# Optimization experiments

Hardware: AMD Instinct MI355X
Metric: run time of the kernel (lower is better)

Reference implementation:

```python
import jax, jax.numpy as jnp
import numpy as np

H = 16  # hidden_dim
EPS = 1e-5


def _lstm_layer(x, W_ih, W_hh, b_ih, b_hh):
    # x: [B,T,D_in] -> [B,T,H]; PyTorch gate order i,f,g,o
    B = x.shape[0]
    xg = jnp.einsum('btd,gd->btg', x, W_ih) + (b_ih + b_hh)  # [B,T,4H]

    def step(carry, xt):
        h, c = carry
        gates = xt + h @ W_hh.T
        i, f, g, o = jnp.split(gates, 4, axis=-1)
        c = jax.nn.sigmoid(f) * c + jax.nn.sigmoid(i) * jnp.tanh(g)
        h = jax.nn.sigmoid(o) * jnp.tanh(c)
        return (h, c), h

    h0 = jnp.zeros((B, H), x.dtype)
    _, hs = jax.lax.scan(step, (h0, h0), jnp.swapaxes(xg, 0, 1))  # [T,B,H]
    return jnp.swapaxes(hs, 0, 1)


def setup_inputs() -> dict:
    key = jax.random.key(0)
    ks = jax.random.split(key, 20)
    B, T, D, O = 256, 2048, 57, 4
    x = jax.random.normal(ks[0], (B, T, D), dtype=jnp.float32)
    lengths = jnp.maximum(jnp.sort(jax.random.randint(ks[1], (B,), 1, T + 1))[::-1], 1)
    s = 1.0 / np.sqrt(H)
    u = lambda k, shp: jax.random.uniform(k, shp, jnp.float32, -s, s)
    inp = {'x': x, 'lengths': lengths}
    dims_in = [D, H, H]
    for l in range(3):
        inp[f'W_ih{l}'] = u(ks[2 + 4 * l], (4 * H, dims_in[l]))
        inp[f'W_hh{l}'] = u(ks[3 + 4 * l], (4 * H, H))
        inp[f'b_ih{l}'] = u(ks[4 + 4 * l], (4 * H,))
        inp[f'b_hh{l}'] = u(ks[5 + 4 * l], (4 * H,))
    inp['bn_gamma'] = jnp.ones((H,), jnp.float32)
    inp['bn_beta'] = jnp.zeros((H,), jnp.float32)
    inp['fc_w'] = u(ks[14], (O, H))
    inp['fc_b'] = u(ks[15], (O,))
    return inp


def reference(x, lengths, W_ih0, W_hh0, b_ih0, b_hh0, W_ih1, W_hh1, b_ih1, b_hh1,
              W_ih2, W_hh2, b_ih2, b_hh2, bn_gamma, bn_beta, fc_w, fc_b):
    B, T, _ = x.shape
    h = x
    for W_ih, W_hh, b_ih, b_hh in ((W_ih0, W_hh0, b_ih0, b_hh0),
                                    (W_ih1, W_hh1, b_ih1, b_hh1),
                                    (W_ih2, W_hh2, b_ih2, b_hh2)):
        h = _lstm_layer(h, W_ih, W_hh, b_ih, b_hh)
    # pad_packed_sequence: zero out positions past each sequence length
    mask = (jnp.arange(T)[None, :] < lengths[:, None])[:, :, None].astype(h.dtype)
    h = h * mask  # [B,T,H]
    # BatchNorm1d (training mode) over (batch,time) per channel, incl. padding zeros
    mean = jnp.mean(h, axis=(0, 1))
    var = jnp.mean((h - mean) ** 2, axis=(0, 1))
    norm = (h - mean) * jax.lax.rsqrt(var + EPS) * bn_gamma + bn_beta
    return norm @ fc_w.T + fc_b  # [B,T,4]
```

## Files before the change

### kernel.cpp

```cpp
#include <hip/hip_runtime.h>
#include <math.h>

#define TT 2048
#define BBATCH 256
#define DDIM 57
#define NROWS (BBATCH*TT)
#define NF 524288.0f
#define U 8
#define G 4
#define NBUF 8
#define XROWS 64

#define K1 (-1.4426950408889634f)
#define K2 (-2.8853900817779268f)

__device__ __forceinline__ float bcastl(float v, int k) {
  return __uint_as_float((unsigned)__builtin_amdgcn_readlane((int)__float_as_uint(v), k));
}
__device__ __forceinline__ float rcpf(float x) { return __builtin_amdgcn_rcpf(x); }
__device__ __forceinline__ float exp2f_(float x) { return __builtin_amdgcn_exp2f(x); }

template<int PAT>
__device__ __forceinline__ float quadb(float v) {
  return __int_as_float(__builtin_amdgcn_update_dpp(0, __float_as_int(v), PAT, 0xF, 0xF, true));
}

__global__ __launch_bounds__(256) void xg0_gemm_k(
    const float* __restrict__ x, const float* __restrict__ Wih,
    const float* __restrict__ bih, const float* __restrict__ bhh,
    float* __restrict__ xg0)
{
  const int tid = threadIdx.x;
  const int l   = tid & 63;
  const int w   = tid >> 6;
  const int g   = (l & 3) * 16 + (l >> 2);
  const float fac = ((l & 3) == 2) ? K2 : K1;

  __shared__ __align__(16) float xs[XROWS][60];

  float wv[60];
  #pragma unroll
  for (int d = 0; d < 60; ++d) wv[d] = (d < DDIM) ? fac * Wih[g*DDIM + d] : 0.f;
  const float bias = fac * (bih[g] + bhh[g]);

  const int rbase = blockIdx.x * XROWS;
  const float4* xsrc = (const float4*)(x + (size_t)rbase * DDIM);
  #pragma unroll
  for (int it = 0; it < 4; ++it) {
    int i = tid + it*256;
    if (i < 912) {
      float4 v = xsrc[i];
      int f0 = 4*i;
      int r0 = f0/57, d0 = f0 - r0*57;            xs[r0][d0] = v.x;
      int f1 = f0+1, r1 = f1/57, d1 = f1 - r1*57; xs[r1][d1] = v.y;
      int f2 = f0+2, r2 = f2/57, d2 = f2 - r2*57; xs[r2][d2] = v.z;
      int f3 = f0+3, r3 = f3/57, d3 = f3 - r3*57; xs[r3][d3] = v.w;
    }
  }
  if (tid < 192) {
    int r = tid/3, c = 57 + (tid - 3*r);
    xs[r][c] = 0.f;
  }
  __syncthreads();

  #pragma unroll
  for (int rr = 0; rr < 16; ++rr) {
    const int r = w*16 + rr;
    const float4* xr = (const float4*)&xs[r][0];
    float a0 = bias, a1 = 0.f, a2 = 0.f, a3 = 0.f;
    #pragma unroll
    for (int i = 0; i < 15; ++i) {
      float4 v = xr[i];
      a0 += wv[4*i]   * v.x;
      a1 += wv[4*i+1] * v.y;
      a2 += wv[4*i+2] * v.z;
      a3 += wv[4*i+3] * v.w;
    }
    xg0[(size_t)(rbase + r)*64 + l] = (a0 + a1) + (a2 + a3);
  }
}

__global__ __launch_bounds__(192, 1) void lstm_scan_pipe_k(
    const float* __restrict__ xg0,
    const int*   __restrict__ lengths,
    const float* __restrict__ Whh0,
    const float* __restrict__ Wih1, const float* __restrict__ Whh1,
    const float* __restrict__ bih1, const float* __restrict__ bhh1,
    const float* __restrict__ Wih2, const float* __restrict__ Whh2,
    const float* __restrict__ bih2, const float* __restrict__ bhh2,
    float* __restrict__ h2buf, float* __restrict__ partial)
{
  const int tid  = threadIdx.x;
  const int wave = tid >> 6;
  const int lane = tid & 63;
  const int gt   = lane & 3;
  const int ch   = lane >> 2;
  const int g    = gt*16 + ch;
  const int b    = blockIdx.x;
  const int len  = lengths[b];
  const bool isg = (gt == 2);
  const float fac = isg ? K2 : K1;
  const float mg = isg ? (2.f*K2) : 1.f;
  const float ag = isg ? (-K2)    : 0.f;

  __shared__ float lds_h0[NBUF][U][16];
  __shared__ float lds_h1[NBUF][U][16];

  float wa[16], wb[16];
  float bias = 0.f;
  if (wave == 0) {
    #pragma unroll
    for (int k = 0; k < 16; ++k) { wb[k] = fac * Whh0[g*16 + k]; wa[k] = 0.f; }
  } else if (wave == 1) {
    #pragma unroll
    for (int k = 0; k < 16; ++k) { wa[k] = fac * Wih1[g*16 + k]; wb[k] = fac * Whh1[g*16 + k]; }
    bias = fac * (bih1[g] + bhh1[g]);
  } else {
    #pragma unroll
    for (int k = 0; k < 16; ++k) { wa[k] = fac * Wih2[g*16 + k]; wb[k] = fac * Whh2[g*16 + k]; }
    bias = fac * (bih2[g] + bhh2[g]);
  }

  float hs = 0.f, csK = 0.f;
  float sum = 0.f, sq = 0.f;
  const int base = b*TT*64 + lane;
  float* __restrict__ h2row = h2buf + (size_t)b*TT*16;

  auto lstm_update = [&](float dot) {
    float s   = rcpf(1.f + exp2f_(dot));
    float act = fmaf(s, mg, ag);
    float gi = quadb<0x00>(act);
    float gf = quadb<0x55>(act);
    float gg = quadb<0xAA>(act);
    float go = quadb<0xFF>(act);
    float go2 = go + go;
    csK = fmaf(gf, csK, gg * gi);
    float r = rcpf(1.f + exp2f_(csK));
    hs = fmaf(go2, r, -go);
  };
  auto owndot = [&](float seed) {
    float hb[16];
    #pragma unroll
    for (int k = 0; k < 16; ++k) hb[k] = bcastl(hs, 4*k);
    float a0 = seed, a1 = 0.f, a2 = 0.f, a3 = 0.f;
    #pragma unroll
    for (int k = 0; k < 16; k += 4) {
      a0 += wb[k]   * hb[k];
      a1 += wb[k+1] * hb[k+1];
      a2 += wb[k+2] * hb[k+2];
      a3 += wb[k+3] * hb[k+3];
    }
    return (a0 + a1) + (a2 + a3);
  };
  auto indot = [&](const float* hin) {
    float a0 = bias, a1 = 0.f, a2 = 0.f, a3 = 0.f;
    #pragma unroll
    for (int k = 0; k < 16; k += 4) {
      a0 += wa[k]   * hin[k];
      a1 += wa[k+1] * hin[k+1];
      a2 += wa[k+2] * hin[k+2];
      a3 += wa[k+3] * hin[k+3];
    }
    return (a0 + a1) + (a2 + a3);
  };

  const int NS = (len + U - 1) / U;
  const int E  = (NS + 2*G - 1) / G + 1;

  float cur[U], nxt[U];
  if (wave == 0) {
    #pragma unroll
    for (int j = 0; j < U; ++j) cur[j] = xg0[base + j*64];
    #pragma unroll
    for (int j = 0; j < U; ++j) {
      int ip = U + j; ip = ip > TT-1 ? TT-1 : ip;
      nxt[j] = xg0[base + ip*64];
    }
  }

  for (int e = 0; e < E; ++e) {
    #pragma unroll 1
    for (int q = 0; q < G; ++q) {
      const int tw = G*e + q;
      if (wave == 0) {
        const int t = tw;
        if (t < NS) {
          const int p = t & (NBUF-1);
          float ld[U];
          #pragma unroll
          for (int j = 0; j < U; ++j) {
            int ip = (t + 2)*U + j; ip = ip > TT-1 ? TT-1 : ip;
            ld[j] = xg0[base + ip*64];
          }
          #pragma unroll
          for (int j = 0; j < U; ++j) {
            lstm_update(owndot(cur[j]));
            if (gt == 0) lds_h0[p][j][ch] = hs;
          }
          #pragma unroll
          for (int j = 0; j < U; ++j) { cur[j] = nxt[j]; nxt[j] = ld[j]; }
        }
      } else if (wave == 1) {
        const int t = tw - G;
        if (t >= 0 && t < NS) {
          const int p = t & (NBUF-1);
          float xin[U];
          #pragma unroll
          for (int j = 0; j < U; ++j) {
            const float4* hp = (const float4*)&lds_h0[p][j][0];
            float4 h0v = hp[0], h1v = hp[1], h2v = hp[2], h3v = hp[3];
            float hin[16] = {h0v.x,h0v.y,h0v.z,h0v.w, h1v.x,h1v.y,h1v.z,h1v.w,
                             h2v.x,h2v.y,h2v.z,h2v.w, h3v.x,h3v.y,h3v.z,h3v.w};
            xin[j] = indot(hin);
          }
          #pragma unroll
          for (int j = 0; j < U; ++j) {
            lstm_update(owndot(xin[j]));
            if (gt == 0) lds_h1[p][j][ch] = hs;
          }
        }
      } else {
        const int t = tw - 2*G;
        if (t >= 0 && t < NS) {
          const int p = t & (NBUF-1);
          float xin[U];
          #pragma unroll
          for (int j = 0; j < U; ++j) {
            const float4* hp = (const float4*)&lds_h1[p][j][0];
            float4 h0v = hp[0], h1v = hp[1], h2v = hp[2], h3v = hp[3];
            float hin[16] = {h0v.x,h0v.y,h0v.z,h0v.w, h1v.x,h1v.y,h1v.z,h1v.w,
                             h2v.x,h2v.y,h2v.z,h2v.w, h3v.x,h3v.y,h3v.z,h3v.w};
            xin[j] = indot(hin);
          }
          #pragma unroll
          for (int j = 0; j < U; ++j) {
            lstm_update(owndot(xin[j]));
            const int ts = t*U + j;
            if (ts < len) {
              if (gt == 0) h2row[ts*16 + ch] = hs;
              sum += hs; sq += hs*hs;
            }
          }
        }
      }
    }
    __syncthreads();
  }

  for (int idx = len*16 + tid; idx < TT*16; idx += 192)
    h2row[idx] = 0.f;

  if (wave == 2 && gt == 0) {
    partial[b*32 + ch]      = sum;
    partial[b*32 + 16 + ch] = sq;
  }
}

__global__ __launch_bounds__(256) void finalize_k(
    const float* __restrict__ partial,
    const float* __restrict__ gamma, const float* __restrict__ beta,
    const float* __restrict__ fcw, const float* __restrict__ fcb,
    const float* __restrict__ h2buf, float* __restrict__ out)
{
  const int tid = threadIdx.x;
  __shared__ float red[8][32];
  __shared__ float coef_s[68];

  const int c = tid & 31, chunk = tid >> 5;
  float acc = 0.f;
  #pragma unroll 4
  for (int bb = chunk; bb < BBATCH; bb += 8)
    acc += partial[bb*32 + c];
  red[chunk][c] = acc;
  __syncthreads();
  if (tid < 32) {
    float tot = 0.f;
    #pragma unroll
    for (int k = 0; k < 8; ++k) tot += red[k][tid];
    red[0][tid] = tot;
  }
  __syncthreads();
  if (tid < 64) {
    const int o = tid >> 4, c2 = tid & 15;
    const float inv_n = 1.0f / NF;
    float mean = red[0][c2] * inv_n;
    float var  = red[0][16 + c2] * inv_n - mean*mean;
    float s  = gamma[c2] * rsqrtf(var + 1e-5f);
    float tb = beta[c2] - mean * s;
    float woc = fcw[o*16 + c2];
    coef_s[tid] = s * woc;
    float term = tb * woc;
    #pragma unroll
    for (int off = 1; off < 16; off <<= 1) term += __shfl_xor(term, off, 16);
    if (c2 == 0) coef_s[64 + o] = fcb[o] + term;
  }
  __syncthreads();

  const int r = blockIdx.x * 256 + tid;
  const float4* hp = (const float4*)(h2buf + (size_t)r * 16);
  float4 v0 = hp[0], v1 = hp[1], v2 = hp[2], v3 = hp[3];
  float hv[16] = {v0.x,v0.y,v0.z,v0.w, v1.x,v1.y,v1.z,v1.w,
                  v2.x,v2.y,v2.z,v2.w, v3.x,v3.y,v3.z,v3.w};
  float4 o4;
  float* op = &o4.x;
  #pragma unroll
  for (int o = 0; o < 4; ++o) {
    float a = coef_s[64 + o];
    #pragma unroll
    for (int c3 = 0; c3 < 16; ++c3) a += coef_s[o*16 + c3] * hv[c3];
    op[o] = a;
  }
  ((float4*)out)[r] = o4;
}

extern "C" void kernel_launch(void* const* d_in, const int* in_sizes, int n_in,
                              void* d_out, int out_size, void* d_ws, size_t ws_size,
                              hipStream_t stream)
{
  const float* x     = (const float*)d_in[0];
  const int* lengths = (const int*)d_in[1];
  const float* W_ih0 = (const float*)d_in[2];
  const float* W_hh0 = (const float*)d_in[3];
  const float* b_ih0 = (const float*)d_in[4];
  const float* b_hh0 = (const float*)d_in[5];
  const float* W_ih1 = (const float*)d_in[6];
  const float* W_hh1 = (const float*)d_in[7];
  const float* b_ih1 = (const float*)d_in[8];
  const float* b_hh1 = (const float*)d_in[9];
  const float* W_ih2 = (const float*)d_in[10];
  const float* W_hh2 = (const float*)d_in[11];
  const float* b_ih2 = (const float*)d_in[12];
  const float* b_hh2 = (const float*)d_in[13];
  const float* gamma = (const float*)d_in[14];
  const float* beta  = (const float*)d_in[15];
  const float* fcw   = (const float*)d_in[16];
  const float* fcb   = (const float*)d_in[17];
  float* out = (float*)d_out;

  float* ws      = (float*)d_ws;
  float* xg0     = ws;
  float* h2      = ws + 33554432;
  float* partial = ws + 33554432 + 8388608;

  hipLaunchKernelGGL(xg0_gemm_k, dim3(NROWS/XROWS), dim3(256), 0, stream,
                     x, W_ih0, b_ih0, b_hh0, xg0);
  hipLaunchKernelGGL(lstm_scan_pipe_k, dim3(256), dim3(192), 0, stream,
                     xg0, lengths, W_hh0, W_ih1, W_hh1, b_ih1, b_hh1,
                     W_ih2, W_hh2, b_ih2, b_hh2, h2, partial);
  hipLaunchKernelGGL(finalize_k, dim3(2048), dim3(256), 0, stream,
                     partial, gamma, beta, fcw, fcb, h2, out);
}
```

Baseline: 646.1 us.

## Process two batch sequences per block to interleave independent LSTM recurrences

Each scan block now handles two adjacent batch rows (sorted descending lengths), interleaving their independent recurrent updates so one chain's latency can hide behind the other's. The grid is halved to 128 blocks, with duplicated LDS buffers and state registers. This targets the serial dependency latency of the per-step gate chain, at the cost of more registers, fewer blocks (under-using CUs on a 256-CU-class GPU), and branches on the shorter sequence's validity.

```diff
diff --git a/kernel.cpp b/kernel.cpp
--- a/kernel.cpp
+++ b/kernel.cpp
@@ -96,15 +96,19 @@
   const int gt   = lane & 3;
   const int ch   = lane >> 2;
   const int g    = gt*16 + ch;
-  const int b    = blockIdx.x;
-  const int len  = lengths[b];
+  const int b0   = blockIdx.x * 2;
+  const int b1   = b0 + 1;
+  const int len0 = lengths[b0];
+  const int len1 = lengths[b1];
   const bool isg = (gt == 2);
   const float fac = isg ? K2 : K1;
   const float mg = isg ? (2.f*K2) : 1.f;
   const float ag = isg ? (-K2)    : 0.f;
 
-  __shared__ float lds_h0[NBUF][U][16];
-  __shared__ float lds_h1[NBUF][U][16];
+  __shared__ float lds_h0A[NBUF][U][16];
+  __shared__ float lds_h0B[NBUF][U][16];
+  __shared__ float lds_h1A[NBUF][U][16];
+  __shared__ float lds_h1B[NBUF][U][16];
 
   float wa[16], wb[16];
   float bias = 0.f;
@@ -121,12 +125,14 @@
     bias = fac * (bih2[g] + bhh2[g]);
   }
 
-  float hs = 0.f, csK = 0.f;
-  float sum = 0.f, sq = 0.f;
-  const int base = b*TT*64 + lane;
-  float* __restrict__ h2row = h2buf + (size_t)b*TT*16;
-
-  auto lstm_update = [&](float dot) {
+  float hsA = 0.f, csKA = 0.f, hsB = 0.f, csKB = 0.f;
+  float sumA = 0.f, sqA = 0.f, sumB = 0.f, sqB = 0.f;
+  const int baseA = b0*TT*64 + lane;
+  const int baseB = b1*TT*64 + lane;
+  float* __restrict__ h2rowA = h2buf + (size_t)b0*TT*16;
+  float* __restrict__ h2rowB = h2buf + (size_t)b1*TT*16;
+
+  auto lstm_update = [&](float dot, float& hs, float& csK) {
     float s   = rcpf(1.f + exp2f_(dot));
     float act = fmaf(s, mg, ag);
     float gi = quadb<0x00>(act);
@@ -138,7 +144,7 @@
     float r = rcpf(1.f + exp2f_(csK));
     hs = fmaf(go2, r, -go);
   };
-  auto owndot = [&](float seed) {
+  auto owndot = [&](float seed, float hs) {
     float hb[16];
     #pragma unroll
     for (int k = 0; k < 16; ++k) hb[k] = bcastl(hs, 4*k);
@@ -163,18 +169,27 @@
     }
     return (a0 + a1) + (a2 + a3);
   };
-
-  const int NS = (len + U - 1) / U;
-  const int E  = (NS + 2*G - 1) / G + 1;
-
-  float cur[U], nxt[U];
+  auto ldhin = [&](const float* src, float* hin) {
+    const float4* hp = (const float4*)src;
+    float4 h0v = hp[0], h1v = hp[1], h2v = hp[2], h3v = hp[3];
+    hin[0]=h0v.x; hin[1]=h0v.y; hin[2]=h0v.z; hin[3]=h0v.w;
+    hin[4]=h1v.x; hin[5]=h1v.y; hin[6]=h1v.z; hin[7]=h1v.w;
+    hin[8]=h2v.x; hin[9]=h2v.y; hin[10]=h2v.z; hin[11]=h2v.w;
+    hin[12]=h3v.x; hin[13]=h3v.y; hin[14]=h3v.z; hin[15]=h3v.w;
+  };
+
+  const int NS0 = (len0 + U - 1) / U;
+  const int NS1 = (len1 + U - 1) / U;
+  const int E   = (NS0 + 2*G - 1) / G + 1;
+
+  float curA[U], nxtA[U], curB[U], nxtB[U];
   if (wave == 0) {
     #pragma unroll
-    for (int j = 0; j < U; ++j) cur[j] = xg0[base + j*64];
+    for (int j = 0; j < U; ++j) { curA[j] = xg0[baseA + j*64]; curB[j] = xg0[baseB + j*64]; }
     #pragma unroll
     for (int j = 0; j < U; ++j) {
       int ip = U + j; ip = ip > TT-1 ? TT-1 : ip;
-      nxt[j] = xg0[base + ip*64];
+      nxtA[j] = xg0[baseA + ip*64]; nxtB[j] = xg0[baseB + ip*64];
     }
   }
 
@@ -184,61 +199,81 @@
       const int tw = G*e + q;
       if (wave == 0) {
         const int t = tw;
-        if (t < NS) {
+        const bool okA = (t < NS0), okB = (t < NS1);
+        if (okA) {
           const int p = t & (NBUF-1);
-          float ld[U];
+          float ldA[U], ldB[U];
           #pragma unroll
           for (int j = 0; j < U; ++j) {
             int ip = (t + 2)*U + j; ip = ip > TT-1 ? TT-1 : ip;
-            ld[j] = xg0[base + ip*64];
-          }
-          #pragma unroll
-          for (int j = 0; j < U; ++j) {
-            lstm_update(owndot(cur[j]));
-            if (gt == 0) lds_h0[p][j][ch] = hs;
-          }
-          #pragma unroll
-          for (int j = 0; j < U; ++j) { cur[j] = nxt[j]; nxt[j] = ld[j]; }
+            ldA[j] = xg0[baseA + ip*64];
+            if (okB) ldB[j] = xg0[baseB + ip*64];
+          }
+          #pragma unroll
+          for (int j = 0; j < U; ++j) {
+            lstm_update(owndot(curA[j], hsA), hsA, csKA);
+            if (gt == 0) lds_h0A[p][j][ch] = hsA;
+            if (okB) {
+              lstm_update(owndot(curB[j], hsB), hsB, csKB);
+              if (gt == 0) lds_h0B[p][j][ch] = hsB;
+            }
+          }
+          #pragma unroll
+          for (int j = 0; j < U; ++j) {
+            curA[j] = nxtA[j]; nxtA[j] = ldA[j];
+            if (okB) { curB[j] = nxtB[j]; nxtB[j] = ldB[j]; }
+          }
         }
       } else if (wave == 1) {
         const int t = tw - G;
-        if (t >= 0 && t < NS) {
+        const bool okA = (t >= 0 && t < NS0), okB = (t >= 0 && t < NS1);
+        if (okA) {
           const int p = t & (NBUF-1);
-          float xin[U];
-          #pragma unroll
-          for (int j = 0; j < U; ++j) {
-            const float4* hp = (const float4*)&lds_h0[p][j][0];
-            float4 h0v = hp[0], h1v = hp[1], h2v = hp[2], h3v = hp[3];
-            float hin[16] = {h0v.x,h0v.y,h0v.z,h0v.w, h1v.x,h1v.y,h1v.z,h1v.w,
-                             h2v.x,h2v.y,h2v.z,h2v.w, h3v.x,h3v.y,h3v.z,h3v.w};
-            xin[j] = indot(hin);
-          }
-          #pragma unroll
-          for (int j = 0; j < U; ++j) {
-            lstm_update(owndot(xin[j]));
-            if (gt == 0) lds_h1[p][j][ch] = hs;
+          float xinA[U], xinB[U];
+          #pragma unroll
+          for (int j = 0; j < U; ++j) {
+            float hin[16];
+            ldhin(&lds_h0A[p][j][0], hin);
+            xinA[j] = indot(hin);
+            if (okB) { ldhin(&lds_h0B[p][j][0], hin); xinB[j] = indot(hin); }
+          }
+          #pragma unroll
+          for (int j = 0; j < U; ++j) {
+            lstm_update(owndot(xinA[j], hsA), hsA, csKA);
+            if (gt == 0) lds_h1A[p][j][ch] = hsA;
+            if (okB) {
+              lstm_update(owndot(xinB[j], hsB), hsB, csKB);
+              if (gt == 0) lds_h1B[p][j][ch] = hsB;
+            }
           }
         }
       } else {
         const int t = tw - 2*G;
-        if (t >= 0 && t < NS) {
+        const bool okA = (t >= 0 && t < NS0), okB = (t >= 0 && t < NS1);
+        if (okA) {
           const int p = t & (NBUF-1);
-          float xin[U];
-          #pragma unroll
-          for (int j = 0; j < U; ++j) {
-            const float4* hp = (const float4*)&lds_h1[p][j][0];
-            float4 h0v = hp[0], h1v = hp[1], h2v = hp[2], h3v = hp[3];
-            float hin[16] = {h0v.x,h0v.y,h0v.z,h0v.w, h1v.x,h1v.y,h1v.z,h1v.w,
-                             h2v.x,h2v.y,h2v.z,h2v.w, h3v.x,h3v.y,h3v.z,h3v.w};
-            xin[j] = indot(hin);
-          }
-          #pragma unroll
-          for (int j = 0; j < U; ++j) {
-            lstm_update(owndot(xin[j]));
+          float xinA[U], xinB[U];
+          #pragma unroll
+          for (int j = 0; j < U; ++j) {
+            float hin[16];
+            ldhin(&lds_h1A[p][j][0], hin);
+            xinA[j] = indot(hin);
+            if (okB) { ldhin(&lds_h1B[p][j][0], hin); xinB[j] = indot(hin); }
+          }
+          #pragma unroll
+          for (int j = 0; j < U; ++j) {
+            lstm_update(owndot(xinA[j], hsA), hsA, csKA);
             const int ts = t*U + j;
-            if (ts < len) {
-              if (gt == 0) h2row[ts*16 + ch] = hs;
-              sum += hs; sq += hs*hs;
+            if (ts < len0) {
+              if (gt == 0) h2rowA[ts*16 + ch] = hsA;
+              sumA += hsA; sqA += hsA*hsA;
+            }
+            if (okB) {
+              lstm_update(owndot(xinB[j], hsB), hsB, csKB);
+              if (ts < len1) {
+                if (gt == 0) h2rowB[ts*16 + ch] = hsB;
+                sumB += hsB; sqB += hsB*hsB;
+              }
             }
           }
         }
@@ -247,12 +282,14 @@
     __syncthreads();
   }
 
-  for (int idx = len*16 + tid; idx < TT*16; idx += 192)
-    h2row[idx] = 0.f;
+  for (int idx = len0*16 + tid; idx < TT*16; idx += 192) h2rowA[idx] = 0.f;
+  for (int idx = len1*16 + tid; idx < TT*16; idx += 192) h2rowB[idx] = 0.f;
 
   if (wave == 2 && gt == 0) {
-    partial[b*32 + ch]      = sum;
-    partial[b*32 + 16 + ch] = sq;
+    partial[b0*32 + ch]      = sumA;
+    partial[b0*32 + 16 + ch] = sqA;
+    partial[b1*32 + ch]      = sumB;
+    partial[b1*32 + 16 + ch] = sqB;
   }
 }
 
@@ -344,7 +381,7 @@
 
   hipLaunchKernelGGL(xg0_gemm_k, dim3(NROWS/XROWS), dim3(256), 0, stream,
                      x, W_ih0, b_ih0, b_hh0, xg0);
-  hipLaunchKernelGGL(lstm_scan_pipe_k, dim3(256), dim3(192), 0, stream,
+  hipLaunchKernelGGL(lstm_scan_pipe_k, dim3(BBATCH/2), dim3(192), 0, stream,
                      xg0, lengths, W_hh0, W_ih1, W_hh1, b_ih1, b_hh1,
                      W_ih2, W_hh2, b_ih2, b_hh2, h2, partial);
   hipLaunchKernelGGL(finalize_k, dim3(2048), dim3(256), 0, stream,
```

New measurement: 1.121 ms. 73.5% more time.
